# Kernel tuning notes

Measured on AMD Instinct MI355X. Metric: run time of the kernel, lower is better.

Reference implementation:

```python
import jax, jax.numpy as jnp
import numpy as np

DIM = 512
HEADS = 8
DIM_HEAD = 64
ROT_DIM = DIM_HEAD // 2  # RotaryEmbedding(dim_head // 2)
B = 4
N = 8192


def rotate_every_two(x):
    # '... (d j) -> ... d j', j=2 ; (x1, x2) -> (-x2, x1) interleaved back
    x1 = x[..., 0::2]
    x2 = x[..., 1::2]
    return jnp.stack((-x2, x1), axis=-1).reshape(x.shape)


def apply_rotary_emb(freqs, t):
    # freqs: [1,1,n,rot_dim]; rotary on first rot_dim channels, passthrough rest
    rot_dim = freqs.shape[-1]
    t_rot, t_pass = t[..., :rot_dim], t[..., rot_dim:]
    t_rot = t_rot * jnp.cos(freqs) + rotate_every_two(t_rot) * jnp.sin(freqs)
    return jnp.concatenate((t_rot, t_pass), axis=-1)


def rotary_freqs(n):
    # lucidrains RotaryEmbedding(ROT_DIM): inv_freq over ROT_DIM//2, repeated r=2
    inv_freq = 1.0 / (10000.0 ** (jnp.arange(0, ROT_DIM, 2, dtype=jnp.float32) / ROT_DIM))
    f = jnp.arange(n, dtype=jnp.float32)[:, None] * inv_freq[None, :]  # [n, ROT_DIM//2]
    return jnp.repeat(f, 2, axis=-1)  # [n, ROT_DIM]


def setup_inputs() -> dict:
    key = jax.random.key(0)
    ks = jax.random.split(key, 8)
    inner = HEADS * DIM_HEAD
    s = lambda fan_in: 1.0 / np.sqrt(fan_in)
    return {
        "x": jax.random.normal(ks[0], (B, N, DIM), dtype=jnp.float32),
        "w_qkv": jax.random.uniform(ks[1], (DIM, inner * 3), jnp.float32, -s(DIM), s(DIM)),
        "w_q_logits": jax.random.uniform(ks[2], (DIM_HEAD, 1), jnp.float32, -s(DIM_HEAD), s(DIM_HEAD)),
        "w_k_logits": jax.random.uniform(ks[3], (DIM_HEAD // 2, 1), jnp.float32, -s(DIM_HEAD // 2), s(DIM_HEAD // 2)),
        "w_r": jax.random.uniform(ks[4], (DIM_HEAD // 2, DIM_HEAD), jnp.float32, -s(DIM_HEAD // 2), s(DIM_HEAD // 2)),
        "b_r": jax.random.uniform(ks[5], (DIM_HEAD,), jnp.float32, -s(DIM_HEAD // 2), s(DIM_HEAD // 2)),
        "w_out": jax.random.uniform(ks[6], (inner, DIM), jnp.float32, -s(inner), s(inner)),
        "b_out": jax.random.uniform(ks[7], (DIM,), jnp.float32, -s(inner), s(inner)),
    }


def reference(x, w_qkv, w_q_logits, w_k_logits, w_r, b_r, w_out, b_out):
    b, n, _ = x.shape
    h, d = HEADS, DIM_HEAD
    scale = d ** -0.5

    qkv = x @ w_qkv  # [b,n,3*h*d]
    q, k, v = jnp.split(qkv, 3, axis=-1)
    to_bhnd = lambda t: t.reshape(b, n, h, d).transpose(0, 2, 1, 3)
    q, k, v = to_bhnd(q), to_bhnd(k), to_bhnd(v)

    freqs = rotary_freqs(n)[None, None]  # [1,1,n,ROT_DIM]
    q_aggr = apply_rotary_emb(freqs, q)
    k_aggr = apply_rotary_emb(freqs, k)
    v_aggr = v

    q_attn = jax.nn.softmax((q @ w_q_logits)[..., 0] * scale, axis=-1)  # [b,h,n]
    global_q = jnp.einsum('bhn,bhnd->bhd', q_attn, q_aggr)[:, :, None]  # [b,h,1,d]

    kk = (k * global_q).reshape(b, h, n, d // 2, 2).sum(-1)  # sum adjacent pairs -> [b,h,n,d/2]
    k_attn = jax.nn.softmax((kk @ w_k_logits)[..., 0] * scale, axis=-1)
    global_k = jnp.einsum('bhn,bhnd->bhd', k_attn, k_aggr)[:, :, None]  # [b,h,1,d]

    u = (v_aggr * global_k).reshape(b, h, n, d // 2, 2).sum(-1)  # [b,h,n,d/2]
    r = u @ w_r + b_r  # [b,h,n,d]
    r = r + q
    r = r.transpose(0, 2, 1, 3).reshape(b, n, h * d)
    return r @ w_out + b_out
```

## Files before the change

### kernel.cpp

```cpp
#include <hip/hip_runtime.h>
#include <hip/hip_bf16.h>

typedef __attribute__((ext_vector_type(8))) short s16x8;
typedef __attribute__((ext_vector_type(4))) short s16x4;
typedef __attribute__((ext_vector_type(4))) float f32x4;

#define SEQ 8192

__device__ __forceinline__ float bf2f(short s){
  union { unsigned u; float f; } c; c.u = ((unsigned)(unsigned short)s) << 16; return c.f;
}
__device__ __forceinline__ short f2bf(float f){
  __hip_bfloat16 h = __float2bfloat16(f);
  short s; __builtin_memcpy(&s, &h, 2); return s;
}

__device__ __forceinline__ void transpose_body(const float* __restrict__ in, __hip_bfloat16* __restrict__ out,
                                               int R, int C, int bx, int by){
  __shared__ float tile[32][33];
  int c0 = bx*32, r0 = by*32;
  int tx = threadIdx.x & 31, ty = threadIdx.x >> 5;
  #pragma unroll
  for (int i = ty; i < 32; i += 8) tile[i][tx] = in[(size_t)(r0+i)*C + c0 + tx];
  __syncthreads();
  #pragma unroll
  for (int i = ty; i < 32; i += 8) out[(size_t)(c0+i)*R + r0 + tx] = __float2bfloat16(tile[tx][i]);
}

__global__ __launch_bounds__(256) void prep(
    const float* __restrict__ x, __hip_bfloat16* __restrict__ xb, unsigned* __restrict__ tab,
    const float* __restrict__ wqkv, __hip_bfloat16* __restrict__ wqkvT,
    const float* __restrict__ wout, __hip_bfloat16* __restrict__ woutT)
{
  int b = blockIdx.x;
  if (b < 16384){
    int i = b*256 + threadIdx.x;
    float4 v = reinterpret_cast<const float4*>(x)[i];
    s16x4 o = { f2bf(v.x), f2bf(v.y), f2bf(v.z), f2bf(v.w) };
    reinterpret_cast<s16x4*>(xb)[i] = o;
  } else if (b < 18432){
    int idx = (b - 16384)*256 + threadIdx.x;
    int n = idx >> 6, d = idx & 63;
    float c, s;
    if (d < 32){
      float ex = -(float)(d & ~1) / 32.0f;
      float invf = __expf(ex * 9.210340371976184f);
      float f = (float)n * invf;
      c = cosf(f);
      s = sinf(f);
      s = (d & 1) ? s : -s;
    } else { c = 1.f; s = 0.f; }
    tab[idx] = (unsigned)(unsigned short)f2bf(c) | ((unsigned)(unsigned short)f2bf(s) << 16);
  } else if (b < 19200){
    int id = b - 18432;
    transpose_body(wqkv, wqkvT, 512, 1536, id % 48, id / 48);
  } else {
    int id = b - 19200;
    transpose_body(wout, woutT, 512, 512, id % 16, id / 16);
  }
}

template<int MODE>
__global__ __launch_bounds__(512, 4) void gemm128(
    const __hip_bfloat16* __restrict__ A, const __hip_bfloat16* __restrict__ BT,
    int M, int Nn, int K,
    __hip_bfloat16* __restrict__ oQ, __hip_bfloat16* __restrict__ oK, __hip_bfloat16* __restrict__ oV,
    float* __restrict__ oF, const float* __restrict__ bias)
{
  __shared__ __align__(16) char lds[73728];
  const int t = threadIdx.x;
  const int lane = t & 63, wid = t >> 6;
  const int lr = lane & 15, lg = lane >> 4;
  const int wm   = (wid >> 2) * 64;
  const int wn64 = (wid & 3) * 64;

  int nwg = gridDim.x, per = nwg >> 3, wg = blockIdx.x;
  int swz = (wg & 7) * per + (wg >> 3);
  int nblk = Nn >> 8;
  int bm = (swz / nblk) << 7;
  int bn = (swz % nblk) << 8;

  const int NKT = K >> 5;

  const __hip_bfloat16* spp[3];
  int dofs[3];
  #pragma unroll
  for (int i = 0; i < 3; ++i){
    int g = (i == 0) ? t : (t + (i-1)*512);
    int row = g >> 2, ch = g & 3;
    int sch = ch ^ ((row >> 1) & 3);
    spp[i] = (i == 0 ? A + (size_t)(bm + row)*K : BT + (size_t)(bn + row)*K) + sch*8;
    dofs[i] = ((i == 0) ? 0 : 8192) + g*16;
  }
  #define STG(i, kt2, bufo) __builtin_amdgcn_global_load_lds( \
      (const __attribute__((address_space(1))) void*)(spp[i] + (size_t)(kt2)*32), \
      (__attribute__((address_space(3))) void*)(lds + (bufo) + dofs[i]), 16, 0, 0)

  STG(0, 0, 0); STG(1, 0, 0); STG(2, 0, 0);
  STG(0, 1, 24576); STG(1, 1, 24576); STG(2, 1, 24576);

  f32x4 acc[4][4] = {};
  int rOff = 0, sOff = 49152;
  #define SWR(r) ((((r) >> 1) & 3) << 4)

  for (int kt = 0; kt < NKT; ++kt){
    if (kt + 1 < NKT) asm volatile("s_waitcnt vmcnt(3)" ::: "memory");
    else              asm volatile("s_waitcnt vmcnt(0)" ::: "memory");
    __builtin_amdgcn_s_barrier();
    __builtin_amdgcn_sched_barrier(0);
    if (kt + 2 < NKT){ STG(0, kt+2, sOff); STG(1, kt+2, sOff); STG(2, kt+2, sOff); }
    const char* lb = lds + rOff;
    s16x8 af[4], bfr[4];
    #pragma unroll
    for (int f = 0; f < 4; ++f){
      int r = wm + f*16 + lr;
      af[f] = *reinterpret_cast<const s16x8*>(lb + (r << 6) + ((lg << 4) ^ SWR(r)));
    }
    #pragma unroll
    for (int f = 0; f < 4; ++f){
      int r = wn64 + f*16 + lr;
      bfr[f] = *reinterpret_cast<const s16x8*>(lb + 8192 + (r << 6) + ((lg << 4) ^ SWR(r)));
    }
    __builtin_amdgcn_s_setprio(1);
    #pragma unroll
    for (int mi = 0; mi < 4; ++mi)
      #pragma unroll
      for (int ni = 0; ni < 4; ++ni)
        acc[mi][ni] = __builtin_amdgcn_mfma_f32_16x16x32_bf16(bfr[ni], af[mi], acc[mi][ni], 0, 0, 0);
    __builtin_amdgcn_s_setprio(0);
    rOff = (rOff == 49152) ? 0 : rOff + 24576;
    sOff = (sOff == 49152) ? 0 : sOff + 24576;
  }
  __builtin_amdgcn_s_barrier();

  if (MODE == 0){
    char* reg = lds + wid*8192;
    #pragma unroll
    for (int mi = 0; mi < 4; ++mi){
      #pragma unroll
      for (int ni = 0; ni < 4; ++ni){
        int tok = mi*16 + lr;
        int sl = (ni*4 + lg) ^ (tok & 15);
        ushort4 w4;
        w4.x = (unsigned short)f2bf(acc[mi][ni][0]);
        w4.y = (unsigned short)f2bf(acc[mi][ni][1]);
        w4.z = (unsigned short)f2bf(acc[mi][ni][2]);
        w4.w = (unsigned short)f2bf(acc[mi][ni][3]);
        *reinterpret_cast<unsigned long long*>(reg + tok*128 + sl*8) =
            *reinterpret_cast<unsigned long long*>(&w4);
      }
    }
    asm volatile("s_waitcnt lgkmcnt(0)" ::: "memory");
    __builtin_amdgcn_sched_barrier(0);
    int gcol = bn + wn64;
    int ts = gcol >> 9, rem = gcol & 511, h = rem >> 6;
    __hip_bfloat16* dstT = (ts == 0) ? oQ : ((ts == 1) ? oK : oV);
    int tokbase = bm + wm;
    int bb = tokbase >> 13;
    dstT += ((size_t)(bb*8 + h)) << 19;
    #pragma unroll
    for (int p2 = 0; p2 < 8; ++p2){
      int tok = p2*8 + (lane >> 3);
      int l0 = (lane & 7) * 2;
      unsigned long long u0 = *reinterpret_cast<const unsigned long long*>(reg + tok*128 + ((l0 ^ (tok & 15)))*8);
      unsigned long long u1 = *reinterpret_cast<const unsigned long long*>(reg + tok*128 + (((l0+1) ^ (tok & 15)))*8);
      int n = (tokbase + tok) & 8191;
      unsigned long long o2[2] = { u0, u1 };
      *reinterpret_cast<s16x8*>(dstT + ((size_t)n << 6) + (lane & 7)*8) =
          *reinterpret_cast<const s16x8*>(o2);
    }
  } else {
    #pragma unroll
    for (int mi = 0; mi < 4; ++mi){
      #pragma unroll
      for (int ni = 0; ni < 4; ++ni){
        int gc = bn + wn64 + ni*16 + lg*4;
        int gr = bm + wm + mi*16 + lr;
        float4 bv = *reinterpret_cast<const float4*>(bias + gc);
        float4 o;
        o.x = acc[mi][ni][0] + bv.x;
        o.y = acc[mi][ni][1] + bv.y;
        o.z = acc[mi][ni][2] + bv.z;
        o.w = acc[mi][ni][3] + bv.w;
        *reinterpret_cast<float4*>(oF + (size_t)gr*Nn + gc) = o;
      }
    }
  }
  #undef STG
  #undef SWR
}

template<int SRC>
__global__ __launch_bounds__(256) void fused_stats(
    const __hip_bfloat16* __restrict__ T, const float* __restrict__ svec,
    const float* __restrict__ partsIn, const float* __restrict__ wkl,
    const unsigned* __restrict__ tab, float* __restrict__ outp)
{
  int chunk = blockIdx.x, bh = blockIdx.y;
  int t = threadIdx.x, lane = t & 63, w = t >> 6;
  __shared__ float sv[64];
  __shared__ float ev[256];
  __shared__ float redv[4][64];
  __shared__ float rede[4];
  if (t < 64){
    float s;
    if (SRC == 0){
      s = svec[t] * 0.125f;
    } else {
      const float* pp = partsIn;
      float tot = 0.f, g = 0.f;
      #pragma unroll 4
      for (int i = 0; i < 32; ++i){ tot += pp[i*66 + 1]; g += pp[i*66 + 2 + t]; }
      s = (g / tot) * wkl[t >> 1] * 0.125f;
    }
    sv[t] = s;
  }
  __syncthreads();

  int n = chunk*256 + t;
  const __hip_bfloat16* row = T + ((size_t)bh*SEQ + n)*64;
  float s = 0.f;
  #pragma unroll
  for (int dv = 0; dv < 8; ++dv){
    s16x8 v8 = *reinterpret_cast<const s16x8*>(row + dv*8);
    #pragma unroll
    for (int e = 0; e < 8; ++e) s += bf2f(v8[e]) * sv[dv*8 + e];
  }
  ev[t] = __expf(s);
  __syncthreads();

  const short* Tb = reinterpret_cast<const short*>(T + ((size_t)bh*SEQ + chunk*256)*64);
  const unsigned* tabb = tab + (size_t)chunk*256*64;
  int g = lane >> 3, j = lane & 7;
  float acc[8] = {0.f,0.f,0.f,0.f,0.f,0.f,0.f,0.f};
  float se = 0.f;
  int tokw = w*64;
  #pragma unroll
  for (int i = 0; i < 8; ++i){
    int tok = tokw + i*8 + g;
    float e = ev[tok];
    s16x8 v8 = *reinterpret_cast<const s16x8*>(Tb + (size_t)tok*64 + j*8);
    uint4 t0 = *reinterpret_cast<const uint4*>(tabb + (size_t)tok*64 + j*8);
    uint4 t1 = *reinterpret_cast<const uint4*>(tabb + (size_t)tok*64 + j*8 + 4);
    #pragma unroll
    for (int e2 = 0; e2 < 8; ++e2){
      unsigned u = (e2 < 4) ? ((const unsigned*)&t0)[e2] : ((const unsigned*)&t1)[e2-4];
      float c  = bf2f((short)(u & 0xffff));
      float s2 = bf2f((short)(u >> 16));
      float xv = bf2f(v8[e2]);
      float xo = bf2f(v8[e2 ^ 1]);
      acc[e2] += e * (xv*c + xo*s2);
    }
    se += e;
  }
  #pragma unroll
  for (int m = 8; m <= 32; m <<= 1){
    #pragma unroll
    for (int e2 = 0; e2 < 8; ++e2) acc[e2] += __shfl_xor(acc[e2], m, 64);
    se += __shfl_xor(se, m, 64);
  }
  if (lane < 8){
    float4 a0 = { acc[0], acc[1], acc[2], acc[3] };
    float4 a1 = { acc[4], acc[5], acc[6], acc[7] };
    *reinterpret_cast<float4*>(&redv[w][lane*8])     = a0;
    *reinterpret_cast<float4*>(&redv[w][lane*8 + 4]) = a1;
  }
  if (lane == 0) rede[w] = se;
  __syncthreads();
  if (t < 64){
    float* ob = outp + (size_t)(bh*32 + chunk)*66;
    ob[2 + t] = redv[0][t] + redv[1][t] + redv[2][t] + redv[3][t];
    if (t == 0) ob[1] = rede[0] + rede[1] + rede[2] + rede[3];
  }
}

__global__ __launch_bounds__(256) void epilogue_r(
    const __hip_bfloat16* __restrict__ vT, const __hip_bfloat16* __restrict__ qT,
    const float* __restrict__ partsK, const float* __restrict__ wr, const float* __restrict__ br,
    __hip_bfloat16* __restrict__ rb)
{
  int idx = blockIdx.x*256 + threadIdx.x;
  int bh = idx >> 13, nl = idx & 8191;
  int b = bh >> 3, h = bh & 7;
  int t = threadIdx.x;
  __shared__ float sgk[64];
  if (t < 64){
    const float* pp = partsK + (size_t)bh*32*66;
    float tot = 0.f, g = 0.f;
    #pragma unroll 4
    for (int i = 0; i < 32; ++i){ tot += pp[i*66 + 1]; g += pp[i*66 + 2 + t]; }
    sgk[t] = g / tot;
  }
  __syncthreads();

  const __hip_bfloat16* vrow = vT + (size_t)idx*64;
  const __hip_bfloat16* qrow = qT + (size_t)idx*64;
  float u[32];
  #pragma unroll
  for (int dv = 0; dv < 8; ++dv){
    s16x8 v8 = *reinterpret_cast<const s16x8*>(vrow + dv*8);
    #pragma unroll
    for (int e = 0; e < 8; e += 2){
      int d = dv*8 + e;
      u[d >> 1] = bf2f(v8[e])*sgk[d] + bf2f(v8[e+1])*sgk[d+1];
    }
  }
  __hip_bfloat16* rrow = rb + ((size_t)(b*SEQ + nl))*512 + h*64;
  #pragma unroll 2
  for (int dv = 0; dv < 8; ++dv){
    s16x8 q8 = *reinterpret_cast<const s16x8*>(qrow + dv*8);
    s16x8 o8;
    #pragma unroll
    for (int e = 0; e < 8; ++e){
      int d = dv*8 + e;
      float a2 = br[d] + bf2f(q8[e]);
      #pragma unroll
      for (int j = 0; j < 32; ++j) a2 += u[j] * wr[j*64 + d];
      o8[e] = f2bf(a2);
    }
    *reinterpret_cast<s16x8*>(rrow + dv*8) = o8;
  }
}

extern "C" void kernel_launch(void* const* d_in, const int* in_sizes, int n_in,
                              void* d_out, int out_size, void* d_ws, size_t ws_size,
                              hipStream_t stream)
{
  (void)in_sizes; (void)n_in; (void)out_size; (void)ws_size;
  const float* x    = (const float*)d_in[0];
  const float* wqkv = (const float*)d_in[1];
  const float* wql  = (const float*)d_in[2];
  const float* wkl  = (const float*)d_in[3];
  const float* wr   = (const float*)d_in[4];
  const float* br   = (const float*)d_in[5];
  const float* wout = (const float*)d_in[6];
  const float* bout = (const float*)d_in[7];
  float* out = (float*)d_out;

  char* p = (char*)d_ws;
  auto alloc = [&](size_t bytes){ char* r = p; p += (bytes + 255) & ~(size_t)255; return r; };
  __hip_bfloat16* xb    = (__hip_bfloat16*)alloc(33554432);
  __hip_bfloat16* wqkvT = (__hip_bfloat16*)alloc(1572864);
  __hip_bfloat16* woutT = (__hip_bfloat16*)alloc(524288);
  __hip_bfloat16* qT = (__hip_bfloat16*)alloc(33554432);
  __hip_bfloat16* kT = (__hip_bfloat16*)alloc(33554432);
  __hip_bfloat16* vT = (__hip_bfloat16*)alloc(33554432);
  __hip_bfloat16* rb = (__hip_bfloat16*)alloc(33554432);
  unsigned* tab = (unsigned*)alloc(2097152);

  float* partsQ = (float*)xb;
  float* partsK = partsQ + 32*32*66;

  prep<<<19456, 256, 0, stream>>>(x, xb, tab, wqkv, wqkvT, wout, woutT);

  gemm128<0><<<1536, 512, 0, stream>>>(xb, wqkvT, 32768, 1536, 512,
                                       qT, kT, vT, nullptr, nullptr);

  fused_stats<0><<<dim3(32,32), 256, 0, stream>>>(qT, wql, nullptr, nullptr, tab, partsQ);
  fused_stats<1><<<dim3(32,32), 256, 0, stream>>>(kT, nullptr, partsQ, wkl, tab, partsK);

  epilogue_r<<<1024, 256, 0, stream>>>(vT, qT, partsK, wr, br, rb);

  gemm128<1><<<512, 512, 0, stream>>>(rb, woutT, 32768, 512, 512,
                                      nullptr, nullptr, nullptr, out, bout);
}
```

Before: 185.7 us.

## Double-buffer QKV GEMM and shrink epilogue staging to raise occupancy

```diff
diff --git a/kernel.cpp b/kernel.cpp
--- a/kernel.cpp
+++ b/kernel.cpp
@@ -61,13 +61,14 @@
 }
 
 template<int MODE>
-__global__ __launch_bounds__(512, 4) void gemm128(
+__global__ __launch_bounds__(512, MODE == 0 ? 6 : 4) void gemm128(
     const __hip_bfloat16* __restrict__ A, const __hip_bfloat16* __restrict__ BT,
     int M, int Nn, int K,
     __hip_bfloat16* __restrict__ oQ, __hip_bfloat16* __restrict__ oK, __hip_bfloat16* __restrict__ oV,
     float* __restrict__ oF, const float* __restrict__ bias)
 {
-  __shared__ __align__(16) char lds[73728];
+  constexpr int NBUF = (MODE == 0) ? 2 : 3;
+  __shared__ __align__(16) char lds[NBUF * 24576];
   const int t = threadIdx.x;
   const int lane = t & 63, wid = t >> 6;
   const int lr = lane & 15, lg = lane >> 4;
@@ -96,78 +97,108 @@
       (const __attribute__((address_space(1))) void*)(spp[i] + (size_t)(kt2)*32), \
       (__attribute__((address_space(3))) void*)(lds + (bufo) + dofs[i]), 16, 0, 0)
 
-  STG(0, 0, 0); STG(1, 0, 0); STG(2, 0, 0);
-  STG(0, 1, 24576); STG(1, 1, 24576); STG(2, 1, 24576);
-
   f32x4 acc[4][4] = {};
-  int rOff = 0, sOff = 49152;
   #define SWR(r) ((((r) >> 1) & 3) << 4)
 
-  for (int kt = 0; kt < NKT; ++kt){
-    if (kt + 1 < NKT) asm volatile("s_waitcnt vmcnt(3)" ::: "memory");
-    else              asm volatile("s_waitcnt vmcnt(0)" ::: "memory");
-    __builtin_amdgcn_s_barrier();
-    __builtin_amdgcn_sched_barrier(0);
-    if (kt + 2 < NKT){ STG(0, kt+2, sOff); STG(1, kt+2, sOff); STG(2, kt+2, sOff); }
-    const char* lb = lds + rOff;
-    s16x8 af[4], bfr[4];
-    #pragma unroll
-    for (int f = 0; f < 4; ++f){
-      int r = wm + f*16 + lr;
-      af[f] = *reinterpret_cast<const s16x8*>(lb + (r << 6) + ((lg << 4) ^ SWR(r)));
-    }
-    #pragma unroll
-    for (int f = 0; f < 4; ++f){
-      int r = wn64 + f*16 + lr;
-      bfr[f] = *reinterpret_cast<const s16x8*>(lb + 8192 + (r << 6) + ((lg << 4) ^ SWR(r)));
-    }
-    __builtin_amdgcn_s_setprio(1);
-    #pragma unroll
-    for (int mi = 0; mi < 4; ++mi)
-      #pragma unroll
-      for (int ni = 0; ni < 4; ++ni)
-        acc[mi][ni] = __builtin_amdgcn_mfma_f32_16x16x32_bf16(bfr[ni], af[mi], acc[mi][ni], 0, 0, 0);
-    __builtin_amdgcn_s_setprio(0);
-    rOff = (rOff == 49152) ? 0 : rOff + 24576;
-    sOff = (sOff == 49152) ? 0 : sOff + 24576;
+  if (MODE == 0){
+    STG(0, 0, 0); STG(1, 0, 0); STG(2, 0, 0);
+    for (int kt = 0; kt < NKT; ++kt){
+      asm volatile("s_waitcnt vmcnt(0)" ::: "memory");
+      __builtin_amdgcn_s_barrier();
+      __builtin_amdgcn_sched_barrier(0);
+      int rOff = (kt & 1) * 24576;
+      int sOff = rOff ^ 24576;
+      if (kt + 1 < NKT){ STG(0, kt+1, sOff); STG(1, kt+1, sOff); STG(2, kt+1, sOff); }
+      const char* lb = lds + rOff;
+      s16x8 af[4], bfr[4];
+      #pragma unroll
+      for (int f = 0; f < 4; ++f){
+        int r = wm + f*16 + lr;
+        af[f] = *reinterpret_cast<const s16x8*>(lb + (r << 6) + ((lg << 4) ^ SWR(r)));
+      }
+      #pragma unroll
+      for (int f = 0; f < 4; ++f){
+        int r = wn64 + f*16 + lr;
+        bfr[f] = *reinterpret_cast<const s16x8*>(lb + 8192 + (r << 6) + ((lg << 4) ^ SWR(r)));
+      }
+      __builtin_amdgcn_s_setprio(1);
+      #pragma unroll
+      for (int mi = 0; mi < 4; ++mi)
+        #pragma unroll
+        for (int ni = 0; ni < 4; ++ni)
+          acc[mi][ni] = __builtin_amdgcn_mfma_f32_16x16x32_bf16(bfr[ni], af[mi], acc[mi][ni], 0, 0, 0);
+      __builtin_amdgcn_s_setprio(0);
+    }
+  } else {
+    STG(0, 0, 0); STG(1, 0, 0); STG(2, 0, 0);
+    STG(0, 1, 24576); STG(1, 1, 24576); STG(2, 1, 24576);
+    int rOff = 0, sOff = 49152;
+    for (int kt = 0; kt < NKT; ++kt){
+      if (kt + 1 < NKT) asm volatile("s_waitcnt vmcnt(3)" ::: "memory");
+      else              asm volatile("s_waitcnt vmcnt(0)" ::: "memory");
+      __builtin_amdgcn_s_barrier();
+      __builtin_amdgcn_sched_barrier(0);
+      if (kt + 2 < NKT){ STG(0, kt+2, sOff); STG(1, kt+2, sOff); STG(2, kt+2, sOff); }
+      const char* lb = lds + rOff;
+      s16x8 af[4], bfr[4];
+      #pragma unroll
+      for (int f = 0; f < 4; ++f){
+        int r = wm + f*16 + lr;
+        af[f] = *reinterpret_cast<const s16x8*>(lb + (r << 6) + ((lg << 4) ^ SWR(r)));
+      }
+      #pragma unroll
+      for (int f = 0; f < 4; ++f){
+        int r = wn64 + f*16 + lr;
+        bfr[f] = *reinterpret_cast<const s16x8*>(lb + 8192 + (r << 6) + ((lg << 4) ^ SWR(r)));
+      }
+      __builtin_amdgcn_s_setprio(1);
+      #pragma unroll
+      for (int mi = 0; mi < 4; ++mi)
+        #pragma unroll
+        for (int ni = 0; ni < 4; ++ni)
+          acc[mi][ni] = __builtin_amdgcn_mfma_f32_16x16x32_bf16(bfr[ni], af[mi], acc[mi][ni], 0, 0, 0);
+      __builtin_amdgcn_s_setprio(0);
+      rOff = (rOff == 49152) ? 0 : rOff + 24576;
+      sOff = (sOff == 49152) ? 0 : sOff + 24576;
+    }
   }
   __builtin_amdgcn_s_barrier();
 
   if (MODE == 0){
-    char* reg = lds + wid*8192;
-    #pragma unroll
-    for (int mi = 0; mi < 4; ++mi){
-      #pragma unroll
-      for (int ni = 0; ni < 4; ++ni){
-        int tok = mi*16 + lr;
-        int sl = (ni*4 + lg) ^ (tok & 15);
-        ushort4 w4;
-        w4.x = (unsigned short)f2bf(acc[mi][ni][0]);
-        w4.y = (unsigned short)f2bf(acc[mi][ni][1]);
-        w4.z = (unsigned short)f2bf(acc[mi][ni][2]);
-        w4.w = (unsigned short)f2bf(acc[mi][ni][3]);
-        *reinterpret_cast<unsigned long long*>(reg + tok*128 + sl*8) =
-            *reinterpret_cast<unsigned long long*>(&w4);
-      }
-    }
-    asm volatile("s_waitcnt lgkmcnt(0)" ::: "memory");
-    __builtin_amdgcn_sched_barrier(0);
+    char* reg = lds + wid*2048;
     int gcol = bn + wn64;
     int ts = gcol >> 9, rem = gcol & 511, h = rem >> 6;
     __hip_bfloat16* dstT = (ts == 0) ? oQ : ((ts == 1) ? oK : oV);
     int tokbase = bm + wm;
     int bb = tokbase >> 13;
     dstT += ((size_t)(bb*8 + h)) << 19;
-    #pragma unroll
-    for (int p2 = 0; p2 < 8; ++p2){
-      int tok = p2*8 + (lane >> 3);
-      int l0 = (lane & 7) * 2;
-      unsigned long long u0 = *reinterpret_cast<const unsigned long long*>(reg + tok*128 + ((l0 ^ (tok & 15)))*8);
-      unsigned long long u1 = *reinterpret_cast<const unsigned long long*>(reg + tok*128 + (((l0+1) ^ (tok & 15)))*8);
-      int n = (tokbase + tok) & 8191;
-      unsigned long long o2[2] = { u0, u1 };
-      *reinterpret_cast<s16x8*>(dstT + ((size_t)n << 6) + (lane & 7)*8) =
-          *reinterpret_cast<const s16x8*>(o2);
+    int tp = lane >> 2, s0 = (lane & 3) * 4;
+    #pragma unroll
+    for (int mi = 0; mi < 4; ++mi){
+      #pragma unroll
+      for (int ni = 0; ni < 4; ++ni){
+        int sl = (ni*4 + lg) ^ lr;
+        ushort4 w4;
+        w4.x = (unsigned short)f2bf(acc[mi][ni][0]);
+        w4.y = (unsigned short)f2bf(acc[mi][ni][1]);
+        w4.z = (unsigned short)f2bf(acc[mi][ni][2]);
+        w4.w = (unsigned short)f2bf(acc[mi][ni][3]);
+        *reinterpret_cast<unsigned long long*>(reg + lr*128 + sl*8) =
+            *reinterpret_cast<unsigned long long*>(&w4);
+      }
+      asm volatile("s_waitcnt lgkmcnt(0)" ::: "memory");
+      __builtin_amdgcn_sched_barrier(0);
+      unsigned long long q0 = *reinterpret_cast<const unsigned long long*>(reg + tp*128 + (((s0    ) ^ tp))*8);
+      unsigned long long q1 = *reinterpret_cast<const unsigned long long*>(reg + tp*128 + (((s0 + 1) ^ tp))*8);
+      unsigned long long q2 = *reinterpret_cast<const unsigned long long*>(reg + tp*128 + (((s0 + 2) ^ tp))*8);
+      unsigned long long q3 = *reinterpret_cast<const unsigned long long*>(reg + tp*128 + (((s0 + 3) ^ tp))*8);
+      int n = (tokbase + mi*16 + tp) & 8191;
+      unsigned long long oA[2] = { q0, q1 };
+      unsigned long long oB[2] = { q2, q3 };
+      *reinterpret_cast<s16x8*>(dstT + ((size_t)n << 6) + s0*4)     = *reinterpret_cast<const s16x8*>(oA);
+      *reinterpret_cast<s16x8*>(dstT + ((size_t)n << 6) + s0*4 + 8) = *reinterpret_cast<const s16x8*>(oB);
+      asm volatile("s_waitcnt lgkmcnt(0)" ::: "memory");
+      __builtin_amdgcn_sched_barrier(0);
     }
   } else {
     #pragma unroll
```

After: 544.3 us. +193.2%, slower.
